# Performance work log

Hardware: AMD Instinct MI355X
Metric: run time of the kernel (lower is better)

Reference implementation:

```python
import jax, jax.numpy as jnp
import numpy as np

B, S, D = 4, 2048, 1024
H, DK, DV = 16, 64, 64
EPS = 1e-6


def setup_inputs() -> dict:
    key = jax.random.key(0)
    ks = jax.random.split(key, 7)
    sc = 0.02
    return {
        "q": jax.random.normal(ks[0], (B, S, D), jnp.float32),
        "k": jax.random.normal(ks[1], (B, S, D), jnp.float32),
        "v": jax.random.normal(ks[2], (B, S, D), jnp.float32),
        "Wq": jax.random.normal(ks[3], (D, H * DK), jnp.float32) * sc,
        "Wk": jax.random.normal(ks[4], (D, H * DK), jnp.float32) * sc,
        "Wv": jax.random.normal(ks[5], (D, H * DV), jnp.float32) * sc,
        "Wo": jax.random.normal(ks[6], (H * DV, D), jnp.float32) * sc,
        "ln_gamma": jnp.ones((D,), jnp.float32),
        "ln_beta": jnp.zeros((D,), jnp.float32),
    }


def reference(q, k, v, Wq, Wk, Wv, Wo, ln_gamma, ln_beta):
    residual = q
    # QKV projections -> [b, h, s, d]
    qh = (q @ Wq).reshape(B, S, H, DK).transpose(0, 2, 1, 3)
    kh = (k @ Wk).reshape(B, S, H, DK).transpose(0, 2, 1, 3)
    vh = (v @ Wv).reshape(B, S, H, DV).transpose(0, 2, 1, 3)
    temperature = jnp.sqrt(jnp.float32(DK))
    # scaled dot-product attention (reverse=False, dropout = eval identity)
    scores = jnp.einsum('bhqd,bhkd->bhqk', qh / temperature, kh)
    attn = jax.nn.softmax(scores, axis=-1)
    ctx = jnp.einsum('bhqk,bhkd->bhqd', attn, vh)
    # merge heads and output projection
    ctx = ctx.transpose(0, 2, 1, 3).reshape(B, S, H * DV)
    out = ctx @ Wo + residual
    # LayerNorm eps=1e-6
    mu = out.mean(-1, keepdims=True)
    var = out.var(-1, keepdims=True)
    out = (out - mu) / jnp.sqrt(var + EPS) * ln_gamma + ln_beta
    return out
```

## Files before the change

kernel.cpp:

```cpp
#include <hip/hip_runtime.h>

typedef __bf16 bf16x8 __attribute__((ext_vector_type(8)));
typedef __bf16 bf16x4 __attribute__((ext_vector_type(4)));
typedef float  f32x4  __attribute__((ext_vector_type(4)));

#define MFMA16(a, b, c) __builtin_amdgcn_mfma_f32_16x16x32_bf16(a, b, c, 0, 0, 0)
#define AS1(p) ((__attribute__((address_space(1))) void*)(p))
#define AS3(p) ((__attribute__((address_space(3))) void*)(p))

union U8 { uint u[4]; bf16x8 v; };
union U4 { bf16x4 h[2]; bf16x8 v; };

__device__ inline uint packbf(float a, float b) {
  union { __bf16 h[2]; uint u; } x;
  x.h[0] = (__bf16)a; x.h[1] = (__bf16)b; return x.u;
}

__device__ inline float fast_exp2(float x) {
  float r;
  asm("v_exp_f32 %0, %1" : "=v"(r) : "v"(x));
  return r;
}

__global__ __launch_bounds__(256) void cvt3_kernel(const float* __restrict__ q,
                                                   const float* __restrict__ k,
                                                   const float* __restrict__ v,
                                                   __bf16* __restrict__ out, int n4) {
  const int z = blockIdx.y;
  const float* in = z == 0 ? q : (z == 1 ? k : v);
  int i = blockIdx.x * blockDim.x + threadIdx.x;
  if (i < n4) {
    float4 vv = ((const float4*)in)[i];
    bf16x4 o = {(__bf16)vv.x, (__bf16)vv.y, (__bf16)vv.z, (__bf16)vv.w};
    *(bf16x4*)(out + (size_t)z * n4 * 4 + (size_t)i * 4) = o;
  }
}

__global__ void wtrans_kernel(const float* __restrict__ in, __bf16* __restrict__ out) {
  __shared__ __bf16 t[64][65];
  int bx = blockIdx.x * 64, by = blockIdx.y * 64;
  int tx = threadIdx.x;
  for (int ty = threadIdx.y; ty < 64; ty += 4)
    t[ty][tx] = (__bf16)in[(size_t)(by + ty) * 1024 + bx + tx];
  __syncthreads();
  for (int ty = threadIdx.y; ty < 64; ty += 4)
    out[(size_t)(bx + ty) * 1024 + by + tx] = t[tx][ty];
}

template <int SWAP, int MODE>
__device__ __forceinline__ void gemm_body(const __bf16* __restrict__ A,
                                          const __bf16* __restrict__ BT,
                                          __bf16* __restrict__ Cb,
                                          float* __restrict__ Cf,
                                          const float* __restrict__ resid,
                                          float scale, __bf16* As, __bf16* Bs) {
  const int K = 1024, N = 1024;
  const int t = threadIdx.x, l = t & 63, w = t >> 6;
  const int lr = l & 15, lg = l >> 4;
  const int brow = blockIdx.y * 128, bcol = blockIdx.x * 128;
  const int wr = w >> 1, wc = w & 1;
  f32x4 acc[4][4] = {};

  const int srow = w * 16 + (l >> 2);
  const int scol = (l & 3) * 8;
  const __bf16* Ag = A + (size_t)(brow + srow) * K + scol;
  const __bf16* Bg = BT + (size_t)(bcol + srow) * K + scol;
  __bf16* Asw = As + w * 512;
  __bf16* Bsw = Bs + w * 512;

  for (int k0 = 0; k0 < K; k0 += 32) {
    __builtin_amdgcn_global_load_lds(AS1(Ag + k0), AS3(Asw), 16, 0, 0);
    __builtin_amdgcn_global_load_lds(AS1(Ag + k0 + (size_t)64 * K), AS3(Asw + 2048), 16, 0, 0);
    __builtin_amdgcn_global_load_lds(AS1(Bg + k0), AS3(Bsw), 16, 0, 0);
    __builtin_amdgcn_global_load_lds(AS1(Bg + k0 + (size_t)64 * K), AS3(Bsw + 2048), 16, 0, 0);
    __syncthreads();
    bf16x8 a[4], b[4];
#pragma unroll
    for (int m = 0; m < 4; ++m)
      a[m] = *(const bf16x8*)(As + (wr * 64 + m * 16 + lr) * 32 + lg * 8);
#pragma unroll
    for (int n = 0; n < 4; ++n)
      b[n] = *(const bf16x8*)(Bs + (wc * 64 + n * 16 + lr) * 32 + lg * 8);
#pragma unroll
    for (int m = 0; m < 4; ++m)
#pragma unroll
      for (int n = 0; n < 4; ++n)
        acc[m][n] = SWAP ? MFMA16(b[n], a[m], acc[m][n])
                         : MFMA16(a[m], b[n], acc[m][n]);
    __syncthreads();
  }

  if (MODE == 3) {
    const int r0 = brow + wr * 64 + lg * 4;
    const int c0 = bcol + wc * 64 + lr;
#pragma unroll
    for (int m = 0; m < 4; ++m)
#pragma unroll
      for (int n = 0; n < 4; ++n) {
        const int dg = c0 + n * 16;
        const int tok = r0 + m * 16;
        bf16x4 pk4;
#pragma unroll
        for (int r = 0; r < 4; ++r) pk4[r] = (__bf16)acc[m][n][r];
        size_t idx = ((size_t)((tok >> 11) * 16 + (dg >> 6)) * 64 + (dg & 63)) * 2048 + (tok & 2047);
        *(bf16x4*)(Cb + idx) = pk4;
      }
  } else {
    const int row0 = brow + wr * 64 + lr;
    const int col0 = bcol + wc * 64 + lg * 4;
#pragma unroll
    for (int m = 0; m < 4; ++m)
#pragma unroll
      for (int n = 0; n < 4; ++n) {
        size_t idx = (size_t)(row0 + m * 16) * N + col0 + n * 16;
        if (MODE == 0) {
          bf16x4 pk4;
#pragma unroll
          for (int r = 0; r < 4; ++r) pk4[r] = (__bf16)(acc[m][n][r] * scale);
          *(bf16x4*)(Cb + idx) = pk4;
        } else {
          float4 rv = *(const float4*)(resid + idx);
          float4 ov = {acc[m][n][0] + rv.x, acc[m][n][1] + rv.y,
                       acc[m][n][2] + rv.z, acc[m][n][3] + rv.w};
          *(float4*)(Cf + idx) = ov;
        }
      }
  }
}

__global__ __launch_bounds__(256) void gemm_qkv_kernel(
    const __bf16* __restrict__ A0, const __bf16* __restrict__ B0, __bf16* __restrict__ C0,
    const __bf16* __restrict__ A1, const __bf16* __restrict__ B1, __bf16* __restrict__ C1,
    const __bf16* __restrict__ A2, const __bf16* __restrict__ B2, __bf16* __restrict__ C2) {
  __shared__ __bf16 As[128 * 32];
  __shared__ __bf16 Bs[128 * 32];
  const int z = blockIdx.z;
  if (z == 2)
    gemm_body<0, 3>(A2, B2, C2, nullptr, nullptr, 1.0f, As, Bs);
  else if (z == 0)
    gemm_body<1, 0>(A0, B0, C0, nullptr, nullptr, 0.1803368801111244f, As, Bs);
  else
    gemm_body<1, 0>(A1, B1, C1, nullptr, nullptr, 1.0f, As, Bs);
}

__global__ __launch_bounds__(256) void gemm_out_kernel(
    const __bf16* __restrict__ A, const __bf16* __restrict__ BT,
    float* __restrict__ Cf, const float* __restrict__ resid) {
  __shared__ __bf16 As[128 * 32];
  __shared__ __bf16 Bs[128 * 32];
  gemm_body<1, 1>(A, BT, nullptr, Cf, resid, 1.0f, As, Bs);
}

__global__ __launch_bounds__(512) void attn_kernel(const __bf16* __restrict__ Qh,
                                                   const __bf16* __restrict__ Kh,
                                                   const __bf16* __restrict__ VhT,
                                                   __bf16* __restrict__ Ctx) {
  __shared__ __bf16 Vbuf[2 * 8192];
  const int t = threadIdx.x, l = t & 63, w = t >> 6;
  const int lr = l & 15, lg = l >> 4;
  const int bh = blockIdx.y;
  const size_t base = (size_t)(bh >> 4) * (2048 * 1024) + (size_t)(bh & 15) * 64;
  const int q0 = blockIdx.x * 256 + w * 32;

  bf16x8 aq[2][2];
#pragma unroll
  for (int nq = 0; nq < 2; ++nq)
#pragma unroll
    for (int kc = 0; kc < 2; ++kc)
      aq[nq][kc] = *(const bf16x8*)(Qh + base + (size_t)(q0 + nq * 16 + lr) * 1024 + kc * 32 + lg * 8);

  bf16x8 ones;
#pragma unroll
  for (int j = 0; j < 8; ++j) ones[j] = (__bf16)1.0f;

  f32x4 o[4][2] = {};
  f32x4 osum[2] = {};

  const int l8 = l & 7, lrow = l >> 3;
  const __bf16* vsrc = VhT + (size_t)bh * 131072 + (size_t)(w * 8 + lrow) * 2048 + ((l8 ^ lrow) * 8);

  const int xorm = (l8) << 4;
  int vo[2][2];
#pragma unroll
  for (int kc = 0; kc < 2; ++kc)
#pragma unroll
    for (int h = 0; h < 2; ++h)
      vo[kc][h] = lr * 128 + ((kc * 64 + h * 32 + lg * 8) ^ xorm);

#pragma unroll
  for (int h2 = 0; h2 < 2; ++h2)
    __builtin_amdgcn_global_load_lds(AS1(vsrc + h2 * 64), AS3(Vbuf + h2 * 4096 + w * 512), 16, 0, 0);
  __syncthreads();

  for (int tt = 0; tt < 16; ++tt) {
    const __bf16* Vcur = Vbuf + (tt & 1) * 8192;
    __bf16* Vn = Vbuf + ((tt + 1) & 1) * 8192;
    const int kvn = ((tt + 1) & 15) * 128;

#pragma unroll
    for (int h2 = 0; h2 < 2; ++h2)
      __builtin_amdgcn_global_load_lds(AS1(vsrc + kvn + h2 * 64), AS3(Vn + h2 * 4096 + w * 512), 16, 0, 0);

#pragma unroll
    for (int h2 = 0; h2 < 2; ++h2) {
      const int kv0 = tt * 128 + h2 * 64;
      const __bf16* Vb = Vcur + h2 * 4096;

      bf16x8 kf[4][2];
#pragma unroll
      for (int mkv = 0; mkv < 4; ++mkv)
#pragma unroll
        for (int kc = 0; kc < 2; ++kc)
          kf[mkv][kc] = *(const bf16x8*)(Kh + base + (size_t)(kv0 + mkv * 16 + lr) * 1024 + kc * 32 + lg * 8);

      f32x4 s[2][4];
      __builtin_amdgcn_s_setprio(1);
#pragma unroll
      for (int nq = 0; nq < 2; ++nq)
#pragma unroll
        for (int mkv = 0; mkv < 4; ++mkv) {
          f32x4 acc = {};
          acc = MFMA16(kf[mkv][0], aq[nq][0], acc);
          acc = MFMA16(kf[mkv][1], aq[nq][1], acc);
          s[nq][mkv] = acc;
        }
      __builtin_amdgcn_s_setprio(0);

      uint pk[2][4][2];
#pragma unroll
      for (int nq = 0; nq < 2; ++nq)
#pragma unroll
        for (int mkv = 0; mkv < 4; ++mkv) {
          float p0 = fast_exp2(s[nq][mkv][0]);
          float p1 = fast_exp2(s[nq][mkv][1]);
          float p2 = fast_exp2(s[nq][mkv][2]);
          float p3 = fast_exp2(s[nq][mkv][3]);
          pk[nq][mkv][0] = packbf(p0, p1);
          pk[nq][mkv][1] = packbf(p2, p3);
        }

      __builtin_amdgcn_s_setprio(1);
#pragma unroll
      for (int kc = 0; kc < 2; ++kc) {
        U8 pf[2];
#pragma unroll
        for (int nq = 0; nq < 2; ++nq) {
          pf[nq].u[0] = pk[nq][2 * kc][0];
          pf[nq].u[1] = pk[nq][2 * kc][1];
          pf[nq].u[2] = pk[nq][2 * kc + 1][0];
          pf[nq].u[3] = pk[nq][2 * kc + 1][1];
          osum[nq] = MFMA16(ones, pf[nq].v, osum[nq]);
        }
#pragma unroll
        for (int md = 0; md < 4; ++md) {
          U4 vf;
          vf.h[0] = *(const bf16x4*)((const char*)Vb + md * 2048 + vo[kc][0]);
          vf.h[1] = *(const bf16x4*)((const char*)Vb + md * 2048 + vo[kc][1]);
#pragma unroll
          for (int nq = 0; nq < 2; ++nq)
            o[md][nq] = MFMA16(vf.v, pf[nq].v, o[md][nq]);
        }
      }
      __builtin_amdgcn_s_setprio(0);
    }

    __syncthreads();
  }

  float rinv[2] = {1.f / osum[0][0], 1.f / osum[1][0]};
#pragma unroll
  for (int md = 0; md < 4; ++md)
#pragma unroll
    for (int nq = 0; nq < 2; ++nq) {
      bf16x4 pk4;
#pragma unroll
      for (int r = 0; r < 4; ++r) pk4[r] = (__bf16)(o[md][nq][r] * rinv[nq]);
      *(bf16x4*)(Ctx + base + (size_t)(q0 + nq * 16 + lr) * 1024 + md * 16 + lg * 4) = pk4;
    }
}

__global__ __launch_bounds__(256) void ln_kernel(const float* __restrict__ x,
                                                 const float* __restrict__ g,
                                                 const float* __restrict__ bta,
                                                 float* __restrict__ out) {
  __shared__ float sred[4], s2red[4];
  const int row = blockIdx.x, t = threadIdx.x;
  float4 v = ((const float4*)(x + (size_t)row * 1024))[t];
  float s = v.x + v.y + v.z + v.w;
  float s2 = v.x * v.x + v.y * v.y + v.z * v.z + v.w * v.w;
#pragma unroll
  for (int mask = 1; mask < 64; mask <<= 1) {
    s += __shfl_xor(s, mask);
    s2 += __shfl_xor(s2, mask);
  }
  if ((t & 63) == 0) { sred[t >> 6] = s; s2red[t >> 6] = s2; }
  __syncthreads();
  s = sred[0] + sred[1] + sred[2] + sred[3];
  s2 = s2red[0] + s2red[1] + s2red[2] + s2red[3];
  float mu = s * (1.f / 1024.f);
  float inv = rsqrtf(s2 * (1.f / 1024.f) - mu * mu + 1e-6f);
  float4 gv = ((const float4*)g)[t];
  float4 bv = ((const float4*)bta)[t];
  float4 ov;
  ov.x = (v.x - mu) * inv * gv.x + bv.x;
  ov.y = (v.y - mu) * inv * gv.y + bv.y;
  ov.z = (v.z - mu) * inv * gv.z + bv.z;
  ov.w = (v.w - mu) * inv * gv.w + bv.w;
  ((float4*)(out + (size_t)row * 1024))[t] = ov;
}

extern "C" void kernel_launch(void* const* d_in, const int* in_sizes, int n_in,
                              void* d_out, int out_size, void* d_ws, size_t ws_size,
                              hipStream_t stream) {
  const float* q  = (const float*)d_in[0];
  const float* k  = (const float*)d_in[1];
  const float* v  = (const float*)d_in[2];
  const float* Wq = (const float*)d_in[3];
  const float* Wk = (const float*)d_in[4];
  const float* Wv = (const float*)d_in[5];
  const float* Wo = (const float*)d_in[6];
  const float* g  = (const float*)d_in[7];
  const float* bt = (const float*)d_in[8];
  float* out = (float*)d_out;

  const int NTOK = 4 * 2048;
  const int NEL = NTOK * 1024;

  __bf16* qb  = (__bf16*)d_ws;
  __bf16* kb  = qb + NEL;
  __bf16* vb  = kb + NEL;
  __bf16* WqT = vb + NEL;
  __bf16* WkT = WqT + 1024 * 1024;
  __bf16* WvT = WkT + 1024 * 1024;
  __bf16* WoT = WvT + 1024 * 1024;
  __bf16* Qh  = WoT + 1024 * 1024;
  __bf16* Kh  = Qh + NEL;
  __bf16* VhT = Kh + NEL;
  __bf16* ctx = qb;
  float*  ao  = (float*)kb;

  cvt3_kernel<<<dim3(NEL / 1024, 3), 256, 0, stream>>>(q, k, v, qb, NEL / 4);

  dim3 wtb(64, 4), wtg(16, 16);
  wtrans_kernel<<<wtg, wtb, 0, stream>>>(Wq, WqT);
  wtrans_kernel<<<wtg, wtb, 0, stream>>>(Wk, WkT);
  wtrans_kernel<<<wtg, wtb, 0, stream>>>(Wv, WvT);
  wtrans_kernel<<<wtg, wtb, 0, stream>>>(Wo, WoT);

  gemm_qkv_kernel<<<dim3(1024 / 128, NTOK / 128, 3), 256, 0, stream>>>(
      qb, WqT, Qh, kb, WkT, Kh, vb, WvT, VhT);

  attn_kernel<<<dim3(2048 / 256, 64), 512, 0, stream>>>(Qh, Kh, VhT, ctx);

  gemm_out_kernel<<<dim3(1024 / 128, NTOK / 128), 256, 0, stream>>>(ctx, WoT, ao, q);

  ln_kernel<<<NTOK, 256, 0, stream>>>(ao, g, bt, out);
}
```

Baseline: 443.3 us.

## Deepen GEMM K-tile to 64 with swizzled LDS, remap blocks for XCD locality

The GEMM main loop now stages a 64-wide K slice per barrier pair instead of 32, halving synchronisation count. An XOR swizzle on the LDS columns avoids bank conflicts on the wider rows. Block indices in the QKV, output and attention kernels are remapped so neighbouring tiles land on the same XCD for L2 reuse. The attention kernel also gains an occupancy hint in its launch bounds. This doubles the LDS footprint per GEMM block, which may reduce occupancy.

```diff
diff --git a/kernel.cpp b/kernel.cpp
--- a/kernel.cpp
+++ b/kernel.cpp
@@ -53,40 +53,50 @@
                                           __bf16* __restrict__ Cb,
                                           float* __restrict__ Cf,
                                           const float* __restrict__ resid,
-                                          float scale, __bf16* As, __bf16* Bs) {
+                                          float scale, __bf16* As, __bf16* Bs,
+                                          int brow, int bcol) {
   const int K = 1024, N = 1024;
   const int t = threadIdx.x, l = t & 63, w = t >> 6;
   const int lr = l & 15, lg = l >> 4;
-  const int brow = blockIdx.y * 128, bcol = blockIdx.x * 128;
   const int wr = w >> 1, wc = w & 1;
   f32x4 acc[4][4] = {};
 
-  const int srow = w * 16 + (l >> 2);
-  const int scol = (l & 3) * 8;
+  const int srow = w * 8 + (l >> 3);
+  const int scol = ((l & 7) ^ (l >> 3)) * 8;
   const __bf16* Ag = A + (size_t)(brow + srow) * K + scol;
   const __bf16* Bg = BT + (size_t)(bcol + srow) * K + scol;
   __bf16* Asw = As + w * 512;
   __bf16* Bsw = Bs + w * 512;
 
-  for (int k0 = 0; k0 < K; k0 += 32) {
-    __builtin_amdgcn_global_load_lds(AS1(Ag + k0), AS3(Asw), 16, 0, 0);
-    __builtin_amdgcn_global_load_lds(AS1(Ag + k0 + (size_t)64 * K), AS3(Asw + 2048), 16, 0, 0);
-    __builtin_amdgcn_global_load_lds(AS1(Bg + k0), AS3(Bsw), 16, 0, 0);
-    __builtin_amdgcn_global_load_lds(AS1(Bg + k0 + (size_t)64 * K), AS3(Bsw + 2048), 16, 0, 0);
+  const int rba = (wr * 64 + lr) * 128;
+  const int rbb = (wc * 64 + lr) * 128;
+  int coff[2];
+  coff[0] = (lg * 16) ^ ((lr & 7) << 4);
+  coff[1] = (64 + lg * 16) ^ ((lr & 7) << 4);
+
+  for (int k0 = 0; k0 < K; k0 += 64) {
+#pragma unroll
+    for (int p = 0; p < 4; ++p) {
+      __builtin_amdgcn_global_load_lds(AS1(Ag + k0 + (size_t)(p * 32) * K), AS3(Asw + p * 2048), 16, 0, 0);
+      __builtin_amdgcn_global_load_lds(AS1(Bg + k0 + (size_t)(p * 32) * K), AS3(Bsw + p * 2048), 16, 0, 0);
+    }
     __syncthreads();
-    bf16x8 a[4], b[4];
-#pragma unroll
-    for (int m = 0; m < 4; ++m)
-      a[m] = *(const bf16x8*)(As + (wr * 64 + m * 16 + lr) * 32 + lg * 8);
-#pragma unroll
-    for (int n = 0; n < 4; ++n)
-      b[n] = *(const bf16x8*)(Bs + (wc * 64 + n * 16 + lr) * 32 + lg * 8);
-#pragma unroll
-    for (int m = 0; m < 4; ++m)
+#pragma unroll
+    for (int kk = 0; kk < 2; ++kk) {
+      bf16x8 a[4], b[4];
+#pragma unroll
+      for (int m = 0; m < 4; ++m)
+        a[m] = *(const bf16x8*)((const char*)As + rba + m * 2048 + coff[kk]);
 #pragma unroll
       for (int n = 0; n < 4; ++n)
-        acc[m][n] = SWAP ? MFMA16(b[n], a[m], acc[m][n])
-                         : MFMA16(a[m], b[n], acc[m][n]);
+        b[n] = *(const bf16x8*)((const char*)Bs + rbb + n * 2048 + coff[kk]);
+#pragma unroll
+      for (int m = 0; m < 4; ++m)
+#pragma unroll
+        for (int n = 0; n < 4; ++n)
+          acc[m][n] = SWAP ? MFMA16(b[n], a[m], acc[m][n])
+                           : MFMA16(a[m], b[n], acc[m][n]);
+    }
     __syncthreads();
   }
 
@@ -132,35 +142,44 @@
     const __bf16* __restrict__ A0, const __bf16* __restrict__ B0, __bf16* __restrict__ C0,
     const __bf16* __restrict__ A1, const __bf16* __restrict__ B1, __bf16* __restrict__ C1,
     const __bf16* __restrict__ A2, const __bf16* __restrict__ B2, __bf16* __restrict__ C2) {
-  __shared__ __bf16 As[128 * 32];
-  __shared__ __bf16 Bs[128 * 32];
-  const int z = blockIdx.z;
+  __shared__ __bf16 As[128 * 64];
+  __shared__ __bf16 Bs[128 * 64];
+  const int lin = blockIdx.x + (blockIdx.y << 3) + (blockIdx.z << 9);
+  const int swz = (lin & 7) * 192 + (lin >> 3);
+  const int z = swz >> 9;
+  const int rem = swz & 511;
+  const int brow = (rem >> 3) * 128, bcol = (rem & 7) * 128;
   if (z == 2)
-    gemm_body<0, 3>(A2, B2, C2, nullptr, nullptr, 1.0f, As, Bs);
+    gemm_body<0, 3>(A2, B2, C2, nullptr, nullptr, 1.0f, As, Bs, brow, bcol);
   else if (z == 0)
-    gemm_body<1, 0>(A0, B0, C0, nullptr, nullptr, 0.1803368801111244f, As, Bs);
+    gemm_body<1, 0>(A0, B0, C0, nullptr, nullptr, 0.1803368801111244f, As, Bs, brow, bcol);
   else
-    gemm_body<1, 0>(A1, B1, C1, nullptr, nullptr, 1.0f, As, Bs);
+    gemm_body<1, 0>(A1, B1, C1, nullptr, nullptr, 1.0f, As, Bs, brow, bcol);
 }
 
 __global__ __launch_bounds__(256) void gemm_out_kernel(
     const __bf16* __restrict__ A, const __bf16* __restrict__ BT,
     float* __restrict__ Cf, const float* __restrict__ resid) {
-  __shared__ __bf16 As[128 * 32];
-  __shared__ __bf16 Bs[128 * 32];
-  gemm_body<1, 1>(A, BT, nullptr, Cf, resid, 1.0f, As, Bs);
-}
-
-__global__ __launch_bounds__(512) void attn_kernel(const __bf16* __restrict__ Qh,
-                                                   const __bf16* __restrict__ Kh,
-                                                   const __bf16* __restrict__ VhT,
-                                                   __bf16* __restrict__ Ctx) {
+  __shared__ __bf16 As[128 * 64];
+  __shared__ __bf16 Bs[128 * 64];
+  const int lin = blockIdx.x + (blockIdx.y << 3);
+  const int swz = (lin & 7) * 64 + (lin >> 3);
+  const int brow = (swz >> 3) * 128, bcol = (swz & 7) * 128;
+  gemm_body<1, 1>(A, BT, nullptr, Cf, resid, 1.0f, As, Bs, brow, bcol);
+}
+
+__global__ __launch_bounds__(512, 4) void attn_kernel(const __bf16* __restrict__ Qh,
+                                                      const __bf16* __restrict__ Kh,
+                                                      const __bf16* __restrict__ VhT,
+                                                      __bf16* __restrict__ Ctx) {
   __shared__ __bf16 Vbuf[2 * 8192];
   const int t = threadIdx.x, l = t & 63, w = t >> 6;
   const int lr = l & 15, lg = l >> 4;
-  const int bh = blockIdx.y;
+  const int lin = blockIdx.x + (blockIdx.y << 3);
+  const int swz = (lin & 7) * 64 + (lin >> 3);
+  const int bh = swz >> 3;
+  const int q0 = (swz & 7) * 256 + w * 32;
   const size_t base = (size_t)(bh >> 4) * (2048 * 1024) + (size_t)(bh & 15) * 64;
-  const int q0 = blockIdx.x * 256 + w * 32;
 
   bf16x8 aq[2][2];
 #pragma unroll
```

After: 424.0 us. 4.4% less time.
